# Kernel optimization log

Hardware: AMD Instinct MI355X
Metric: run time of the kernel (lower is better)

Reference implementation:

```python
import math
import jax, jax.numpy as jnp
import numpy as np

B, S, D, H = 4, 1024, 768, 12  # batch, seq, hidden, heads (ViT-Base)
HD = D // H                     # head size = 64
EPS = 1e-12                     # F.normalize eps


def setup_inputs() -> dict:
    key = jax.random.key(0)
    ks = jax.random.split(key, 7)
    s = 0.02
    return {
        "hidden_states": jax.random.normal(ks[0], (B, S, D), dtype=jnp.float32),
        "Wq": jax.random.normal(ks[1], (D, D), dtype=jnp.float32) * s,
        "bq": jax.random.normal(ks[2], (D,), dtype=jnp.float32) * s,
        "Wv": jax.random.normal(ks[3], (D, D), dtype=jnp.float32) * s,
        "bv": jax.random.normal(ks[4], (D,), dtype=jnp.float32) * s,
        "Wo": jax.random.normal(ks[5], (D, D), dtype=jnp.float32) * s,
        "bo": jax.random.normal(ks[6], (D,), dtype=jnp.float32) * s,
    }


def _split_heads(x):
    # [B,S,D] -> [B,H,S,hd]
    b, s, _ = x.shape
    return x.reshape(b, s, H, HD).transpose(0, 2, 1, 3)


def reference(hidden_states, Wq, bq, Wv, bv, Wo, bo):
    b, s, d_model = hidden_states.shape
    # Linear layers (torch Linear: x @ W^T + b; here W stored already transposed)
    mixed_q = hidden_states @ Wq + bq          # key == query in this module
    mixed_v = hidden_states @ Wv + bv
    q = _split_heads(mixed_q)                  # [B,H,S,hd]
    v = _split_heads(mixed_v)                  # [B,H,S,hd]

    # symmetric self-attention (Q @ Q^T)
    scores = jnp.einsum("bhsd,bhtd->bhst", q, q) / math.sqrt(HD)
    probs1 = jax.nn.softmax(scores, axis=-1)                 # [B,H,S,S]
    probs = 0.5 * (probs1 + probs1.transpose(0, 1, 3, 2))    # symmetrize

    # F.normalize(value_layer, dim=2): L2-normalize along the SEQUENCE axis
    vnorm = jnp.maximum(jnp.sqrt(jnp.sum(v * v, axis=2, keepdims=True)), EPS)
    V = v / vnorm                                            # [B,H,S,hd]

    # random-walk Laplacian: D^{-1}(D - P) = I - P / rowsum  (diag structure exploited,
    # same math as diag_embed + matmul in the original)
    dvec = probs.sum(axis=3)                                 # [B,H,S]
    Pn = probs / dvec[..., :, None]                          # D^{-1} P
    LrwV = V - jnp.einsum("bhst,bhtd->bhsd", Pn, V)          # L_rw @ V

    # trace( sum_{b,h} V^T L_rw V ) = sum over all (b,h,s,d) of V * (L_rw V)
    denom = jnp.float32(HD * H * b)
    tr = jnp.abs(jnp.sum(V * LrwV)) / denom

    # orthogonality regularizer: sum (V^T V - I)^2
    VtV = jnp.einsum("bhsd,bhse->bhde", V, V)                # [B,H,hd,hd]
    regular_term = jnp.sum((VtV - jnp.eye(HD, dtype=V.dtype)) ** 2) / denom

    # context = P @ V  (is_last=False)
    ctx = jnp.einsum("bhst,bhtd->bhsd", probs, v)
    ctx = ctx.transpose(0, 2, 1, 3).reshape(b, s, d_model)
    attention_output = ctx @ Wo + bo                         # dropout = identity (p=0)
    return (attention_output, tr, regular_term, mixed_q, mixed_q)
```

## Files before the change

### kernel.cpp

```cpp
#include <hip/hip_runtime.h>
#include <math.h>

constexpr float SCALE = 0.125f;

typedef __attribute__((ext_vector_type(8))) short bf8;
typedef __attribute__((ext_vector_type(8))) unsigned short u16x8;
typedef __attribute__((ext_vector_type(4))) float f32x4;

static __device__ __forceinline__ unsigned short f2bf(float f) {
    unsigned int u = __float_as_uint(f);
    u += 0x7fffu + ((u >> 16) & 1u);
    return (unsigned short)(u >> 16);
}
static __device__ __forceinline__ float bf2f(unsigned short h) {
    return __uint_as_float(((unsigned int)h) << 16);
}
static __device__ __forceinline__ bf8 ld8(const unsigned short* p) {
    return *reinterpret_cast<const bf8*>(p);
}
static __device__ __forceinline__ unsigned int cvtpk(float lo, float hi) {
    unsigned int r;
    asm("v_cvt_pk_bf16_f32 %0, %1, %2" : "=v"(r) : "v"(lo), "v"(hi));
    return r;
}

__global__ __launch_bounds__(256)
void k_prep(const float* __restrict__ Wq, const float* __restrict__ Wv,
            unsigned short* __restrict__ WTq, unsigned short* __restrict__ WTv)
{
    __shared__ unsigned short T[64 * 72];
    const int bid = blockIdx.x;
    const bool isQ = (bid < 144);
    const int lb = isQ ? bid : bid - 144;
    const float* __restrict__ W = isQ ? Wq : Wv;
    unsigned short* __restrict__ WT = isQ ? WTq : WTv;
    const int n0 = (lb % 12) * 64;
    const int k0 = (lb / 12) * 64;
    const int tid = threadIdx.x;
    const int r  = tid >> 2;
    const int c0 = (tid & 3) * 16;
    const float* src = &W[(size_t)(k0 + r) * 768 + n0 + c0];
    #pragma unroll
    for (int q = 0; q < 4; ++q) {
        const float4 v = *reinterpret_cast<const float4*>(src + q * 4);
        uint2 pk;
        pk.x = cvtpk(v.x, v.y);
        pk.y = cvtpk(v.z, v.w);
        *reinterpret_cast<uint2*>(&T[r * 72 + c0 + q * 4]) = pk;
    }
    __syncthreads();
    const int n  = tid >> 2;
    const int kc = (tid & 3) * 16;
    u16x8 o0, o1;
    #pragma unroll
    for (int i = 0; i < 8; ++i) o0[i] = T[(kc + i) * 72 + n];
    #pragma unroll
    for (int i = 0; i < 8; ++i) o1[i] = T[(kc + 8 + i) * 72 + n];
    unsigned short* dst = WT + (size_t)(n0 + n) * 768 + k0 + kc;
    *reinterpret_cast<u16x8*>(dst)     = o0;
    *reinterpret_cast<u16x8*>(dst + 8) = o1;
}

__global__ __launch_bounds__(256)
void k_gemm_qv(const float* __restrict__ X,
               const unsigned short* __restrict__ WTq,
               const unsigned short* __restrict__ WTv,
               const float* __restrict__ bq, const float* __restrict__ bv,
               float* __restrict__ mq1, float* __restrict__ mq2,
               unsigned short* __restrict__ qb, unsigned short* __restrict__ mvb)
{
    __shared__ unsigned short As[64 * 136];
    __shared__ unsigned short Bs[128 * 136];
    const int m0 = blockIdx.x * 64;
    const bool isQ = (blockIdx.y < 6);
    const int n0 = (isQ ? blockIdx.y : blockIdx.y - 6) * 128;
    const unsigned short* __restrict__ WT = isQ ? WTq : WTv;
    const float* __restrict__ bias = isQ ? bq : bv;
    const int tid = threadIdx.x;
    const int wave = tid >> 6, lane = tid & 63, lm = lane & 15, lg = lane >> 4;
    const int wn = wave;

    f32x4 acc[4][2];
    #pragma unroll
    for (int mi = 0; mi < 4; ++mi)
        #pragma unroll
        for (int ni = 0; ni < 2; ++ni) acc[mi][ni] = (f32x4){0.f, 0.f, 0.f, 0.f};

    float4 ar[8];
    u16x8  br[8];

    #pragma unroll
    for (int it = 0; it < 8; ++it) {
        const int idx = tid + it * 256;
        ar[it] = *reinterpret_cast<const float4*>(
            &X[(size_t)(m0 + (idx >> 5)) * 768 + (idx & 31) * 4]);
        br[it] = *reinterpret_cast<const u16x8*>(
            &WT[(size_t)(n0 + (idx >> 4)) * 768 + (idx & 15) * 8]);
    }
    #pragma unroll
    for (int it = 0; it < 8; ++it) {
        const int idx = tid + it * 256;
        uint2 pk;
        pk.x = cvtpk(ar[it].x, ar[it].y);
        pk.y = cvtpk(ar[it].z, ar[it].w);
        *reinterpret_cast<uint2*>(&As[(idx >> 5) * 136 + (idx & 31) * 4]) = pk;
        *reinterpret_cast<u16x8*>(&Bs[(idx >> 4) * 136 + (idx & 15) * 8]) = br[it];
    }
    __syncthreads();

    for (int step = 0; step < 6; ++step) {
        const bool pf = (step < 5);
        if (pf) {
            const int k0 = (step + 1) * 128;
            #pragma unroll
            for (int it = 0; it < 8; ++it) {
                const int idx = tid + it * 256;
                ar[it] = *reinterpret_cast<const float4*>(
                    &X[(size_t)(m0 + (idx >> 5)) * 768 + k0 + (idx & 31) * 4]);
                br[it] = *reinterpret_cast<const u16x8*>(
                    &WT[(size_t)(n0 + (idx >> 4)) * 768 + k0 + (idx & 15) * 8]);
            }
        }
        #pragma unroll
        for (int ks = 0; ks < 4; ++ks) {
            bf8 af[4], bfr[2];
            #pragma unroll
            for (int mi = 0; mi < 4; ++mi)
                af[mi] = *reinterpret_cast<const bf8*>(
                    &As[(mi * 16 + lm) * 136 + ks * 32 + lg * 8]);
            #pragma unroll
            for (int ni = 0; ni < 2; ++ni)
                bfr[ni] = *reinterpret_cast<const bf8*>(
                    &Bs[(wn * 32 + ni * 16 + lm) * 136 + ks * 32 + lg * 8]);
            #pragma unroll
            for (int mi = 0; mi < 4; ++mi)
                #pragma unroll
                for (int ni = 0; ni < 2; ++ni)
                    acc[mi][ni] = __builtin_amdgcn_mfma_f32_16x16x32_bf16(
                        af[mi], bfr[ni], acc[mi][ni], 0, 0, 0);
        }
        __syncthreads();
        if (pf) {
            #pragma unroll
            for (int it = 0; it < 8; ++it) {
                const int idx = tid + it * 256;
                uint2 pk;
                pk.x = cvtpk(ar[it].x, ar[it].y);
                pk.y = cvtpk(ar[it].z, ar[it].w);
                *reinterpret_cast<uint2*>(&As[(idx >> 5) * 136 + (idx & 31) * 4]) = pk;
                *reinterpret_cast<u16x8*>(&Bs[(idx >> 4) * 136 + (idx & 15) * 8]) = br[it];
            }
        }
        __syncthreads();
    }
    #pragma unroll
    for (int ni = 0; ni < 2; ++ni) {
        const int c = n0 + wn * 32 + ni * 16 + lm;
        const float bcol = bias[c];
        #pragma unroll
        for (int mi = 0; mi < 4; ++mi)
            #pragma unroll
            for (int j = 0; j < 4; ++j) {
                const int r = m0 + mi * 16 + lg * 4 + j;
                const float v = acc[mi][ni][j] + bcol;
                const size_t off = (size_t)r * 768 + c;
                if (isQ) {
                    mq1[off] = v;
                    mq2[off] = v;
                    qb[off]  = f2bf(v);
                } else {
                    mvb[off] = f2bf(v);
                }
            }
    }
}

__global__ __launch_bounds__(256)
void k_gemm_one(const unsigned short* __restrict__ Xb,
                const unsigned short* __restrict__ WT,
                const float* __restrict__ bias, float* __restrict__ out,
                const float* __restrict__ t1p, const float* __restrict__ t2p,
                const float* __restrict__ regp, float* __restrict__ out_tr,
                float* __restrict__ out_reg)
{
    __shared__ unsigned short As[64 * 136];
    __shared__ unsigned short Bs[64 * 136];
    __shared__ float R1[256];
    __shared__ float R2[256];
    __shared__ float R3[256];
    const int tid = threadIdx.x;

    if (blockIdx.x == 768) {
        float s1 = 0.f, s2 = 0.f, s3 = 0.f;
        for (int i = tid; i < 768; i += 256) s2 += t2p[i];
        if (tid < 48) { s1 = t1p[tid]; s3 = regp[tid]; }
        R1[tid] = s1; R2[tid] = s2; R3[tid] = s3;
        __syncthreads();
        for (int w = 128; w >= 1; w >>= 1) {
            if (tid < w) { R1[tid] += R1[tid + w]; R2[tid] += R2[tid + w]; R3[tid] += R3[tid + w]; }
            __syncthreads();
        }
        if (tid == 0) {
            *out_tr  = fabsf(R1[0] - R2[0]) / 3072.f;
            *out_reg = R3[0] / 3072.f;
        }
        return;
    }

    const int m0 = (blockIdx.x & 63) * 64;
    const int n0 = (blockIdx.x >> 6) * 64;
    const int w = tid >> 6, lane = tid & 63, lm = lane & 15, lg = lane >> 4;

    f32x4 acc[4];
    #pragma unroll
    for (int ni = 0; ni < 4; ++ni) acc[ni] = (f32x4){0.f, 0.f, 0.f, 0.f};

    u16x8 ara[4], arb[4];
    #pragma unroll
    for (int it = 0; it < 4; ++it) {
        const int idx = tid + it * 256;
        ara[it] = *reinterpret_cast<const u16x8*>(
            &Xb[(size_t)(m0 + (idx >> 4)) * 768 + (idx & 15) * 8]);
        arb[it] = *reinterpret_cast<const u16x8*>(
            &WT[(size_t)(n0 + (idx >> 4)) * 768 + (idx & 15) * 8]);
    }
    #pragma unroll
    for (int it = 0; it < 4; ++it) {
        const int idx = tid + it * 256;
        *reinterpret_cast<u16x8*>(&As[(idx >> 4) * 136 + (idx & 15) * 8]) = ara[it];
        *reinterpret_cast<u16x8*>(&Bs[(idx >> 4) * 136 + (idx & 15) * 8]) = arb[it];
    }
    __syncthreads();

    for (int step = 0; step < 6; ++step) {
        const bool pf = (step < 5);
        if (pf) {
            const int k0 = (step + 1) * 128;
            #pragma unroll
            for (int it = 0; it < 4; ++it) {
                const int idx = tid + it * 256;
                ara[it] = *reinterpret_cast<const u16x8*>(
                    &Xb[(size_t)(m0 + (idx >> 4)) * 768 + k0 + (idx & 15) * 8]);
                arb[it] = *reinterpret_cast<const u16x8*>(
                    &WT[(size_t)(n0 + (idx >> 4)) * 768 + k0 + (idx & 15) * 8]);
            }
        }
        #pragma unroll
        for (int ks = 0; ks < 4; ++ks) {
            const bf8 af = *reinterpret_cast<const bf8*>(
                &As[(w * 16 + lm) * 136 + ks * 32 + lg * 8]);
            #pragma unroll
            for (int ni = 0; ni < 4; ++ni) {
                const bf8 bfr = *reinterpret_cast<const bf8*>(
                    &Bs[(ni * 16 + lm) * 136 + ks * 32 + lg * 8]);
                acc[ni] = __builtin_amdgcn_mfma_f32_16x16x32_bf16(af, bfr, acc[ni], 0, 0, 0);
            }
        }
        __syncthreads();
        if (pf) {
            #pragma unroll
            for (int it = 0; it < 4; ++it) {
                const int idx = tid + it * 256;
                *reinterpret_cast<u16x8*>(&As[(idx >> 4) * 136 + (idx & 15) * 8]) = ara[it];
                *reinterpret_cast<u16x8*>(&Bs[(idx >> 4) * 136 + (idx & 15) * 8]) = arb[it];
            }
        }
        __syncthreads();
    }
    #pragma unroll
    for (int ni = 0; ni < 4; ++ni) {
        const int c = n0 + ni * 16 + lm;
        const float bcol = bias[c];
        #pragma unroll
        for (int j = 0; j < 4; ++j) {
            const int r = m0 + w * 16 + lg * 4 + j;
            out[(size_t)r * 768 + c] = acc[ni][j] + bcol;
        }
    }
}

__global__ __launch_bounds__(256)
void k_pass1T(const unsigned short* __restrict__ qb,
              const unsigned short* __restrict__ mvb,
              unsigned short* __restrict__ vT,
              float* __restrict__ a, float* __restrict__ nrmp)
{
    __shared__ __align__(16) unsigned short Kb[2][128 * 72];
    const int bid = blockIdx.x;
    const int st = (bid >> 3) & 15;
    const int bh = (bid & 7) + 8 * (bid >> 7);
    const int b = bh / 12, h = bh % 12;
    const int s0 = st * 64;
    const int tid = threadIdx.x;
    const int w = tid >> 6, lane = tid & 63, lm = lane & 15, lg = lane >> 4;
    const size_t qoff = (size_t)(b * 1024) * 768 + h * 64;

    {
        const int r  = tid >> 2;
        const int c0 = (tid & 3) * 16;
        const unsigned short* src = mvb + (size_t)(b * 1024 + s0 + r) * 768 + h * 64 + c0;
        const u16x8 x0 = *reinterpret_cast<const u16x8*>(src);
        const u16x8 x1 = *reinterpret_cast<const u16x8*>(src + 8);
        *reinterpret_cast<u16x8*>(&Kb[0][r * 72 + c0])     = x0;
        *reinterpret_cast<u16x8*>(&Kb[0][r * 72 + c0 + 8]) = x1;
        __syncthreads();
        const int dd  = tid >> 2;
        const int sc0 = (tid & 3) * 16;
        u16x8 o0, o1;
        float ps = 0.f;
        #pragma unroll
        for (int k = 0; k < 8; ++k) {
            o0[k] = Kb[0][(sc0 + k) * 72 + dd];
            const float v = bf2f(o0[k]);
            ps = fmaf(v, v, ps);
        }
        #pragma unroll
        for (int k = 0; k < 8; ++k) {
            o1[k] = Kb[0][(sc0 + 8 + k) * 72 + dd];
            const float v = bf2f(o1[k]);
            ps = fmaf(v, v, ps);
        }
        ps += __shfl_xor(ps, 1);
        ps += __shfl_xor(ps, 2);
        if ((tid & 3) == 0) nrmp[(size_t)(bh * 16 + st) * 64 + dd] = ps;
        unsigned short* dst = vT + (size_t)bh * 65536 + (size_t)dd * 1024 + s0 + sc0;
        *reinterpret_cast<u16x8*>(dst)     = o0;
        *reinterpret_cast<u16x8*>(dst + 8) = o1;
        __syncthreads();
    }

    const unsigned short* srow_p = qb + qoff + (size_t)(s0 + 16 * w + lm) * 768;
    const bf8 qs0 = ld8(srow_p + 8 * lg);
    const bf8 qs1 = ld8(srow_p + 32 + 8 * lg);
    const f32x4 z = {0.f, 0.f, 0.f, 0.f};
    float r = 0.f;

    u16x8 kr[4];
    #pragma unroll
    for (int it = 0; it < 4; ++it) {
        const int idx = tid + it * 256;
        kr[it] = *reinterpret_cast<const u16x8*>(
            qb + qoff + (size_t)(idx >> 3) * 768 + (idx & 7) * 8);
    }
    #pragma unroll
    for (int it = 0; it < 4; ++it) {
        const int idx = tid + it * 256;
        *reinterpret_cast<u16x8*>(&Kb[0][(idx >> 3) * 72 + (idx & 7) * 8]) = kr[it];
    }
    __syncthreads();
    int cur = 0;

    for (int tt = 0; tt < 8; ++tt) {
        const bool pf = (tt < 7);
        if (pf) {
            #pragma unroll
            for (int it = 0; it < 4; ++it) {
                const int idx = tid + it * 256;
                kr[it] = *reinterpret_cast<const u16x8*>(
                    qb + qoff + (size_t)((tt + 1) * 128 + (idx >> 3)) * 768 + (idx & 7) * 8);
            }
        }
        #pragma unroll
        for (int nf = 0; nf < 8; ++nf) {
            const bf8 ka0 = *reinterpret_cast<const bf8*>(
                &Kb[cur][(16 * nf + lm) * 72 + 8 * lg]);
            const bf8 ka1 = *reinterpret_cast<const bf8*>(
                &Kb[cur][(16 * nf + lm) * 72 + 32 + 8 * lg]);
            f32x4 ef = __builtin_amdgcn_mfma_f32_16x16x32_bf16(ka0, qs0, z, 0, 0, 0);
            ef = __builtin_amdgcn_mfma_f32_16x16x32_bf16(ka1, qs1, ef, 0, 0, 0);
            r += __expf(ef[0] * SCALE) + __expf(ef[1] * SCALE)
               + __expf(ef[2] * SCALE) + __expf(ef[3] * SCALE);
        }
        if (pf) {
            #pragma unroll
            for (int it = 0; it < 4; ++it) {
                const int idx = tid + it * 256;
                *reinterpret_cast<u16x8*>(
                    &Kb[cur ^ 1][(idx >> 3) * 72 + (idx & 7) * 8]) = kr[it];
            }
        }
        __syncthreads();
        cur ^= 1;
    }
    r += __shfl_xor(r, 16);
    r += __shfl_xor(r, 32);
    if (lg == 0) a[(size_t)bh * 1024 + s0 + 16 * w + lm] = 1.f / r;
}

__global__ __launch_bounds__(256)
void k_pass2(const unsigned short* __restrict__ qb,
             const unsigned short* __restrict__ vT,
             const unsigned short* __restrict__ mvb,
             const float* __restrict__ a,
             const float* __restrict__ nrmp,
             float* __restrict__ invn_out,
             unsigned short* __restrict__ ctxb,
             float* __restrict__ t2p)
{
    __shared__ __align__(16) unsigned short Kb[2][64 * 72];
    __shared__ __align__(16) unsigned short Vb[2][64 * 72];
    __shared__ __align__(16) unsigned short F_lds[4 * 16 * 72];
    __shared__ float red[256];
    __shared__ float inv_sh[64];
    const int bid = blockIdx.x;
    const int st = (bid >> 3) & 15;
    const int bh = (bid & 7) + 8 * (bid >> 7);
    const int b = bh / 12, h = bh % 12;
    const int s0 = st * 64;
    const int tid = threadIdx.x;
    const int w = tid >> 6, lane = tid & 63, lm = lane & 15, lg = lane >> 4;
    const size_t qoff = (size_t)(b * 1024) * 768 + h * 64;
    const unsigned short* srow_p = qb + qoff + (size_t)(s0 + 16 * w + lm) * 768;
    const bf8 qs0 = ld8(srow_p + 8 * lg);
    const bf8 qs1 = ld8(srow_p + 32 + 8 * lg);
    const unsigned short* vbase = vT + (size_t)bh * 65536;
    const float* abase = a + (size_t)bh * 1024;
    const float a_s = abase[s0 + 16 * w + lm];
    unsigned short* Frow = &F_lds[w * 1152 + lm * 72];
    const f32x4 z = {0.f, 0.f, 0.f, 0.f};
    f32x4 acc[4];
    #pragma unroll
    for (int nf = 0; nf < 4; ++nf) acc[nf] = z;
    float sF = 0.f;
    const int sr = tid >> 2;
    const int sc = (tid & 3) << 4;

    if (tid < 64) {
        float s = 0.f;
        #pragma unroll
        for (int t = 0; t < 16; ++t) s += nrmp[(size_t)(bh * 16 + t) * 64 + tid];
        const float iv = 1.f / fmaxf(sqrtf(s), 1e-12f);
        inv_sh[tid] = iv;
        if (st == 0) invn_out[bh * 64 + tid] = iv;
    }

    u16x8 kr0 = *reinterpret_cast<const u16x8*>(qb + qoff + (size_t)sr * 768 + sc);
    u16x8 kr1 = *reinterpret_cast<const u16x8*>(qb + qoff + (size_t)sr * 768 + sc + 8);
    u16x8 vr0 = *reinterpret_cast<const u16x8*>(vbase + (size_t)sr * 1024 + sc);
    u16x8 vr1 = *reinterpret_cast<const u16x8*>(vbase + (size_t)sr * 1024 + sc + 8);
    *reinterpret_cast<u16x8*>(&Kb[0][sr * 72 + sc])     = kr0;
    *reinterpret_cast<u16x8*>(&Kb[0][sr * 72 + sc + 8]) = kr1;
    *reinterpret_cast<u16x8*>(&Vb[0][sr * 72 + sc])     = vr0;
    *reinterpret_cast<u16x8*>(&Vb[0][sr * 72 + sc + 8]) = vr1;
    __syncthreads();
    int cur = 0;

    for (int tt = 0; tt < 16; ++tt) {
        const int t0 = tt * 64;
        if (tt < 15) {
            const size_t kg = qoff + (size_t)(t0 + 64 + sr) * 768 + sc;
            kr0 = *reinterpret_cast<const u16x8*>(qb + kg);
            kr1 = *reinterpret_cast<const u16x8*>(qb + kg + 8);
            const size_t vg = (size_t)sr * 1024 + t0 + 64 + sc;
            vr0 = *reinterpret_cast<const u16x8*>(vbase + vg);
            vr1 = *reinterpret_cast<const u16x8*>(vbase + vg + 8);
        }
        f32x4 ef[4];
        #pragma unroll
        for (int nf = 0; nf < 4; ++nf) {
            const bf8 ka0 = *reinterpret_cast<const bf8*>(
                &Kb[cur][(16 * nf + lm) * 72 + 8 * lg]);
            const bf8 ka1 = *reinterpret_cast<const bf8*>(
                &Kb[cur][(16 * nf + lm) * 72 + 32 + 8 * lg]);
            ef[nf] = __builtin_amdgcn_mfma_f32_16x16x32_bf16(ka0, qs0, z, 0, 0, 0);
            ef[nf] = __builtin_amdgcn_mfma_f32_16x16x32_bf16(ka1, qs1, ef[nf], 0, 0, 0);
        }
        #pragma unroll
        for (int nf = 0; nf < 4; ++nf) {
            const float4 af = *reinterpret_cast<const float4*>(
                abase + t0 + 16 * nf + 4 * lg);
            const float f0 = __expf(ef[nf][0] * SCALE) * (a_s + af.x);
            const float f1 = __expf(ef[nf][1] * SCALE) * (a_s + af.y);
            const float f2 = __expf(ef[nf][2] * SCALE) * (a_s + af.z);
            const float f3 = __expf(ef[nf][3] * SCALE) * (a_s + af.w);
            sF += (f0 + f1) + (f2 + f3);
            uint2 pk;
            pk.x = cvtpk(f0, f1);
            pk.y = cvtpk(f2, f3);
            *reinterpret_cast<uint2*>(&Frow[16 * nf + 4 * lg]) = pk;
        }
        #pragma unroll
        for (int ks = 0; ks < 2; ++ks) {
            const bf8 fa = *reinterpret_cast<const bf8*>(&Frow[32 * ks + 8 * lg]);
            #pragma unroll
            for (int nf = 0; nf < 4; ++nf) {
                const bf8 vfr = *reinterpret_cast<const bf8*>(
                    &Vb[cur][(16 * nf + lm) * 72 + 32 * ks + 8 * lg]);
                acc[nf] = __builtin_amdgcn_mfma_f32_16x16x32_bf16(fa, vfr, acc[nf], 0, 0, 0);
            }
        }
        if (tt < 15) {
            *reinterpret_cast<u16x8*>(&Kb[cur ^ 1][sr * 72 + sc])     = kr0;
            *reinterpret_cast<u16x8*>(&Kb[cur ^ 1][sr * 72 + sc + 8]) = kr1;
            *reinterpret_cast<u16x8*>(&Vb[cur ^ 1][sr * 72 + sc])     = vr0;
            *reinterpret_cast<u16x8*>(&Vb[cur ^ 1][sr * 72 + sc + 8]) = vr1;
        }
        __syncthreads();
        cur ^= 1;
    }
    sF += __shfl_xor(sF, 16);
    sF += __shfl_xor(sF, 32);

    float t2 = 0.f;
    #pragma unroll
    for (int j = 0; j < 4; ++j) {
        const int srow = s0 + 16 * w + 4 * lg + j;
        const float sFj = __shfl(sF, 4 * lg + j);
        const float rdv = 2.f / sFj;
        const size_t rowoff = (size_t)(b * 1024 + srow) * 768 + h * 64;
        #pragma unroll
        for (int nf = 0; nf < 4; ++nf) {
            const int d = lm + 16 * nf;
            const float iv = inv_sh[d];
            const float cf = 0.5f * acc[nf][j];
            ctxb[rowoff + d] = f2bf(cf);
            const float vv = bf2f(mvb[rowoff + d]);
            t2 = fmaf(vv * cf, iv * iv * rdv, t2);
        }
    }
    red[tid] = t2;
    __syncthreads();
    for (int k = 128; k >= 1; k >>= 1) {
        if (tid < k) red[tid] += red[tid + k];
        __syncthreads();
    }
    if (tid == 0) t2p[bh * 16 + st] = red[0];
}

__global__ __launch_bounds__(256)
void k_regwt(const unsigned short* __restrict__ vT, float* __restrict__ Gpart,
             const float* __restrict__ Wo, unsigned short* __restrict__ WTo)
{
    __shared__ unsigned short T[64 * 72];
    const int bid = blockIdx.x;
    const int tid = threadIdx.x;
    if (bid < 384) {
        const int bh = bid >> 3;
        const int q  = bid & 7;
        const int w = tid >> 6, lane = tid & 63, lm = lane & 15, lg = lane >> 4;
        const unsigned short* base = vT + (size_t)bh * 65536;
        const unsigned short* arowp = base + (size_t)(16 * w + lm) * 1024;
        const f32x4 z = {0.f, 0.f, 0.f, 0.f};
        f32x4 acc[4];
        #pragma unroll
        for (int nf = 0; nf < 4; ++nf) acc[nf] = z;
        #pragma unroll
        for (int kk = 0; kk < 4; ++kk) {
            const int t0 = (q * 4 + kk) * 32 + 8 * lg;
            const bf8 av = ld8(arowp + t0);
            #pragma unroll
            for (int nf = 0; nf < 4; ++nf) {
                const bf8 bv = ld8(base + (size_t)(lm + 16 * nf) * 1024 + t0);
                acc[nf] = __builtin_amdgcn_mfma_f32_16x16x32_bf16(av, bv, acc[nf], 0, 0, 0);
            }
        }
        float* gdst = Gpart + (size_t)(bh * 8 + q) * 4096;
        #pragma unroll
        for (int nf = 0; nf < 4; ++nf) {
            const int d2 = lm + 16 * nf;
            #pragma unroll
            for (int j = 0; j < 4; ++j) {
                const int d1 = 16 * w + 4 * lg + j;
                gdst[d1 * 64 + d2] = acc[nf][j];
            }
        }
    } else {
        const int lb = bid - 384;
        const int n0 = (lb % 12) * 64;
        const int k0 = (lb / 12) * 64;
        const int r  = tid >> 2;
        const int c0 = (tid & 3) * 16;
        const float* src = &Wo[(size_t)(k0 + r) * 768 + n0 + c0];
        #pragma unroll
        for (int q = 0; q < 4; ++q) {
            const float4 v = *reinterpret_cast<const float4*>(src + q * 4);
            uint2 pk;
            pk.x = cvtpk(v.x, v.y);
            pk.y = cvtpk(v.z, v.w);
            *reinterpret_cast<uint2*>(&T[r * 72 + c0 + q * 4]) = pk;
        }
        __syncthreads();
        const int n  = tid >> 2;
        const int kc = (tid & 3) * 16;
        u16x8 o0, o1;
        #pragma unroll
        for (int i = 0; i < 8; ++i) o0[i] = T[(kc + i) * 72 + n];
        #pragma unroll
        for (int i = 0; i < 8; ++i) o1[i] = T[(kc + 8 + i) * 72 + n];
        unsigned short* dst = WTo + (size_t)(n0 + n) * 768 + k0 + kc;
        *reinterpret_cast<u16x8*>(dst)     = o0;
        *reinterpret_cast<u16x8*>(dst + 8) = o1;
    }
}

__global__ __launch_bounds__(256)
void k_regfin(const float* __restrict__ Gpart, const float* __restrict__ invn,
              const float* __restrict__ nrmp,
              float* __restrict__ regp, float* __restrict__ t1p)
{
    const int bh = blockIdx.x;
    const int tid = threadIdx.x;
    float part = 0.f;
    for (int c = tid; c < 4096; c += 256) {
        const int d1 = c >> 6, d2 = c & 63;
        float g = 0.f;
        #pragma unroll
        for (int q = 0; q < 8; ++q)
            g += Gpart[(size_t)(bh * 8 + q) * 4096 + c];
        g *= invn[bh * 64 + d1] * invn[bh * 64 + d2];
        const float diff = g - ((d1 == d2) ? 1.f : 0.f);
        part = fmaf(diff, diff, part);
    }
    float t1l = 0.f;
    if (tid < 64) {
        float s = 0.f;
        #pragma unroll
        for (int t = 0; t < 16; ++t) s += nrmp[(size_t)(bh * 16 + t) * 64 + tid];
        const float iv = invn[bh * 64 + tid];
        t1l = s * iv * iv;
    }
    __shared__ float red[256];
    __shared__ float redT[256];
    red[tid] = part;
    redT[tid] = t1l;
    __syncthreads();
    for (int k = 128; k >= 1; k >>= 1) {
        if (tid < k) { red[tid] += red[tid + k]; redT[tid] += redT[tid + k]; }
        __syncthreads();
    }
    if (tid == 0) { regp[bh] = red[0]; t1p[bh] = redT[0]; }
}

extern "C" void kernel_launch(void* const* d_in, const int* in_sizes, int n_in,
                              void* d_out, int out_size, void* d_ws, size_t ws_size,
                              hipStream_t stream)
{
    const float* X  = (const float*)d_in[0];
    const float* Wq = (const float*)d_in[1];
    const float* bq = (const float*)d_in[2];
    const float* Wv = (const float*)d_in[3];
    const float* bv = (const float*)d_in[4];
    const float* Wo = (const float*)d_in[5];
    const float* bo = (const float*)d_in[6];

    float* out = (float*)d_out;
    float* att = out;
    float* tr  = out + 3145728;
    float* rg  = out + 3145729;
    float* mq1 = out + 3145730;
    float* mq2 = out + 6291458;

    float* ws = (float*)d_ws;
    unsigned short* mvb  = (unsigned short*)(ws);
    unsigned short* WTo  = (unsigned short*)(ws);
    unsigned short* qb   = (unsigned short*)(ws + 1572864);
    float*          Gpart = ws + 1572864;
    unsigned short* vTslot = (unsigned short*)(ws + 3145728);
    unsigned short* WTq  = vTslot;
    unsigned short* WTv  = vTslot + 589824;
    unsigned short* vT   = vTslot;
    unsigned short* ctxb = (unsigned short*)(ws + 4718592);
    float* nrmp = ws + 6291456;
    float* aarr = ws + 6389760;
    float* invn = ws + 6438960;
    float* t1p  = ws + 6442032;
    float* t2p  = ws + 6442080;
    float* regp = ws + 6442848;

    if (ws_size < (size_t)6442896 * sizeof(float)) return;

    k_prep     <<<288,          256, 0, stream>>>(Wq, Wv, WTq, WTv);
    k_gemm_qv  <<<dim3(64, 12), 256, 0, stream>>>(X, WTq, WTv, bq, bv, mq1, mq2, qb, mvb);
    k_pass1T   <<<768,          256, 0, stream>>>(qb, mvb, vT, aarr, nrmp);
    k_pass2    <<<768,          256, 0, stream>>>(qb, vT, mvb, aarr, nrmp, invn, ctxb, t2p);
    k_regwt    <<<528,          256, 0, stream>>>(vT, Gpart, Wo, WTo);
    k_regfin   <<<48,           256, 0, stream>>>(Gpart, invn, nrmp, regp, t1p);
    k_gemm_one <<<769,          256, 0, stream>>>(ctxb, WTo, bo, att,
                                                  t1p, t2p, regp, tr, rg);
}
```

Before: 123.0 us.

## Double-buffer LDS in projection GEMMs with smaller K tiles and more blocks

Both GEMM kernels now use two LDS buffers with a 64-wide K step, so the next tile is written to the other buffer while the current one is consumed. This drops one barrier per iteration. The QV GEMM tile also shrinks from 64x128 to 64x64, doubling the grid to 1536 blocks for better occupancy across CUs. The cost is twice as many K iterations, each with less MFMA work to hide global loads, and less operand reuse per block.

```diff
diff --git a/kernel.cpp b/kernel.cpp
--- a/kernel.cpp
+++ b/kernel.cpp
@@ -69,109 +69,113 @@
                float* __restrict__ mq1, float* __restrict__ mq2,
                unsigned short* __restrict__ qb, unsigned short* __restrict__ mvb)
 {
-    __shared__ unsigned short As[64 * 136];
-    __shared__ unsigned short Bs[128 * 136];
+    __shared__ __align__(16) unsigned short As[2][64 * 72];
+    __shared__ __align__(16) unsigned short Bs[2][64 * 72];
     const int m0 = blockIdx.x * 64;
-    const bool isQ = (blockIdx.y < 6);
-    const int n0 = (isQ ? blockIdx.y : blockIdx.y - 6) * 128;
+    const bool isQ = (blockIdx.y < 12);
+    const int n0 = (isQ ? blockIdx.y : blockIdx.y - 12) * 64;
     const unsigned short* __restrict__ WT = isQ ? WTq : WTv;
     const float* __restrict__ bias = isQ ? bq : bv;
     const int tid = threadIdx.x;
-    const int wave = tid >> 6, lane = tid & 63, lm = lane & 15, lg = lane >> 4;
-    const int wn = wave;
-
-    f32x4 acc[4][2];
-    #pragma unroll
-    for (int mi = 0; mi < 4; ++mi)
-        #pragma unroll
-        for (int ni = 0; ni < 2; ++ni) acc[mi][ni] = (f32x4){0.f, 0.f, 0.f, 0.f};
-
-    float4 ar[8];
-    u16x8  br[8];
-
-    #pragma unroll
-    for (int it = 0; it < 8; ++it) {
+    const int w = tid >> 6, lane = tid & 63, lm = lane & 15, lg = lane >> 4;
+
+    f32x4 acc[4];
+    #pragma unroll
+    for (int ni = 0; ni < 4; ++ni) acc[ni] = (f32x4){0.f, 0.f, 0.f, 0.f};
+
+    float4 ar[4];
+    u16x8  br[2];
+    #pragma unroll
+    for (int it = 0; it < 4; ++it) {
         const int idx = tid + it * 256;
         ar[it] = *reinterpret_cast<const float4*>(
-            &X[(size_t)(m0 + (idx >> 5)) * 768 + (idx & 31) * 4]);
+            &X[(size_t)(m0 + (idx >> 4)) * 768 + (idx & 15) * 4]);
+    }
+    #pragma unroll
+    for (int it = 0; it < 2; ++it) {
+        const int idx = tid + it * 256;
         br[it] = *reinterpret_cast<const u16x8*>(
-            &WT[(size_t)(n0 + (idx >> 4)) * 768 + (idx & 15) * 8]);
-    }
-    #pragma unroll
-    for (int it = 0; it < 8; ++it) {
+            &WT[(size_t)(n0 + (idx >> 3)) * 768 + (idx & 7) * 8]);
+    }
+    #pragma unroll
+    for (int it = 0; it < 4; ++it) {
         const int idx = tid + it * 256;
         uint2 pk;
         pk.x = cvtpk(ar[it].x, ar[it].y);
         pk.y = cvtpk(ar[it].z, ar[it].w);
-        *reinterpret_cast<uint2*>(&As[(idx >> 5) * 136 + (idx & 31) * 4]) = pk;
-        *reinterpret_cast<u16x8*>(&Bs[(idx >> 4) * 136 + (idx & 15) * 8]) = br[it];
+        *reinterpret_cast<uint2*>(&As[0][(idx >> 4) * 72 + (idx & 15) * 4]) = pk;
+    }
+    #pragma unroll
+    for (int it = 0; it < 2; ++it) {
+        const int idx = tid + it * 256;
+        *reinterpret_cast<u16x8*>(&Bs[0][(idx >> 3) * 72 + (idx & 7) * 8]) = br[it];
     }
     __syncthreads();
-
-    for (int step = 0; step < 6; ++step) {
-        const bool pf = (step < 5);
+    int cur = 0;
+
+    for (int step = 0; step < 12; ++step) {
+        const bool pf = (step < 11);
         if (pf) {
-            const int k0 = (step + 1) * 128;
-            #pragma unroll
-            for (int it = 0; it < 8; ++it) {
+            const int k0 = (step + 1) * 64;
+            #pragma unroll
+            for (int it = 0; it < 4; ++it) {
                 const int idx = tid + it * 256;
                 ar[it] = *reinterpret_cast<const float4*>(
-                    &X[(size_t)(m0 + (idx >> 5)) * 768 + k0 + (idx & 31) * 4]);
+                    &X[(size_t)(m0 + (idx >> 4)) * 768 + k0 + (idx & 15) * 4]);
+            }
+            #pragma unroll
+            for (int it = 0; it < 2; ++it) {
+                const int idx = tid + it * 256;
                 br[it] = *reinterpret_cast<const u16x8*>(
-                    &WT[(size_t)(n0 + (idx >> 4)) * 768 + k0 + (idx & 15) * 8]);
-            }
-        }
-        #pragma unroll
-        for (int ks = 0; ks < 4; ++ks) {
-            bf8 af[4], bfr[2];
-            #pragma unroll
-            for (int mi = 0; mi < 4; ++mi)
-                af[mi] = *reinterpret_cast<const bf8*>(
-                    &As[(mi * 16 + lm) * 136 + ks * 32 + lg * 8]);
-            #pragma unroll
-            for (int ni = 0; ni < 2; ++ni)
-                bfr[ni] = *reinterpret_cast<const bf8*>(
-                    &Bs[(wn * 32 + ni * 16 + lm) * 136 + ks * 32 + lg * 8]);
-            #pragma unroll
-            for (int mi = 0; mi < 4; ++mi)
-                #pragma unroll
-                for (int ni = 0; ni < 2; ++ni)
-                    acc[mi][ni] = __builtin_amdgcn_mfma_f32_16x16x32_bf16(
-                        af[mi], bfr[ni], acc[mi][ni], 0, 0, 0);
-        }
-        __syncthreads();
+                    &WT[(size_t)(n0 + (idx >> 3)) * 768 + k0 + (idx & 7) * 8]);
+            }
+        }
+        #pragma unroll
+        for (int ks = 0; ks < 2; ++ks) {
+            const bf8 af = *reinterpret_cast<const bf8*>(
+                &As[cur][(w * 16 + lm) * 72 + ks * 32 + lg * 8]);
+            #pragma unroll
+            for (int ni = 0; ni < 4; ++ni) {
+                const bf8 bfr = *reinterpret_cast<const bf8*>(
+                    &Bs[cur][(ni * 16 + lm) * 72 + ks * 32 + lg * 8]);
+                acc[ni] = __builtin_amdgcn_mfma_f32_16x16x32_bf16(af, bfr, acc[ni], 0, 0, 0);
+            }
+        }
         if (pf) {
             #pragma unroll
-            for (int it = 0; it < 8; ++it) {
+            for (int it = 0; it < 4; ++it) {
                 const int idx = tid + it * 256;
                 uint2 pk;
                 pk.x = cvtpk(ar[it].x, ar[it].y);
                 pk.y = cvtpk(ar[it].z, ar[it].w);
-                *reinterpret_cast<uint2*>(&As[(idx >> 5) * 136 + (idx & 31) * 4]) = pk;
-                *reinterpret_cast<u16x8*>(&Bs[(idx >> 4) * 136 + (idx & 15) * 8]) = br[it];
-            }
-        }
-        __syncthreads();
-    }
-    #pragma unroll
-    for (int ni = 0; ni < 2; ++ni) {
-        const int c = n0 + wn * 32 + ni * 16 + lm;
+                *reinterpret_cast<uint2*>(&As[cur ^ 1][(idx >> 4) * 72 + (idx & 15) * 4]) = pk;
+            }
+            #pragma unroll
+            for (int it = 0; it < 2; ++it) {
+                const int idx = tid + it * 256;
+                *reinterpret_cast<u16x8*>(&Bs[cur ^ 1][(idx >> 3) * 72 + (idx & 7) * 8]) = br[it];
+            }
+        }
+        __syncthreads();
+        cur ^= 1;
+    }
+    #pragma unroll
+    for (int ni = 0; ni < 4; ++ni) {
+        const int c = n0 + ni * 16 + lm;
         const float bcol = bias[c];
         #pragma unroll
-        for (int mi = 0; mi < 4; ++mi)
-            #pragma unroll
-            for (int j = 0; j < 4; ++j) {
-                const int r = m0 + mi * 16 + lg * 4 + j;
-                const float v = acc[mi][ni][j] + bcol;
-                const size_t off = (size_t)r * 768 + c;
-                if (isQ) {
-                    mq1[off] = v;
-                    mq2[off] = v;
-                    qb[off]  = f2bf(v);
-                } else {
-                    mvb[off] = f2bf(v);
-                }
-            }
+        for (int j = 0; j < 4; ++j) {
+            const int r = m0 + w * 16 + lg * 4 + j;
+            const float v = acc[ni][j] + bcol;
+            const size_t off = (size_t)r * 768 + c;
+            if (isQ) {
+                mq1[off] = v;
+                mq2[off] = v;
+                qb[off]  = f2bf(v);
+            } else {
+                mvb[off] = f2bf(v);
+            }
+        }
     }
 }
 
@@ -183,8 +187,8 @@
                 const float* __restrict__ regp, float* __restrict__ out_tr,
                 float* __restrict__ out_reg)
 {
-    __shared__ unsigned short As[64 * 136];
-    __shared__ unsigned short Bs[64 * 136];
+    __shared__ __align__(16) unsigned short As[2][64 * 72];
+    __shared__ __align__(16) unsigned short Bs[2][64 * 72];
     __shared__ float R1[256];
     __shared__ float R2[256];
     __shared__ float R3[256];
@@ -215,57 +219,58 @@
     #pragma unroll
     for (int ni = 0; ni < 4; ++ni) acc[ni] = (f32x4){0.f, 0.f, 0.f, 0.f};
 
-    u16x8 ara[4], arb[4];
-    #pragma unroll
-    for (int it = 0; it < 4; ++it) {
+    u16x8 ara[2], arb[2];
+    #pragma unroll
+    for (int it = 0; it < 2; ++it) {
         const int idx = tid + it * 256;
         ara[it] = *reinterpret_cast<const u16x8*>(
-            &Xb[(size_t)(m0 + (idx >> 4)) * 768 + (idx & 15) * 8]);
+            &Xb[(size_t)(m0 + (idx >> 3)) * 768 + (idx & 7) * 8]);
         arb[it] = *reinterpret_cast<const u16x8*>(
-            &WT[(size_t)(n0 + (idx >> 4)) * 768 + (idx & 15) * 8]);
-    }
-    #pragma unroll
-    for (int it = 0; it < 4; ++it) {
-        const int idx = tid + it * 256;
-        *reinterpret_cast<u16x8*>(&As[(idx >> 4) * 136 + (idx & 15) * 8]) = ara[it];
-        *reinterpret_cast<u16x8*>(&Bs[(idx >> 4) * 136 + (idx & 15) * 8]) = arb[it];
+            &WT[(size_t)(n0 + (idx >> 3)) * 768 + (idx & 7) * 8]);
+    }
+    #pragma unroll
+    for (int it = 0; it < 2; ++it) {
+        const int idx = tid + it * 256;
+        *reinterpret_cast<u16x8*>(&As[0][(idx >> 3) * 72 + (idx & 7) * 8]) = ara[it];
+        *reinterpret_cast<u16x8*>(&Bs[0][(idx >> 3) * 72 + (idx & 7) * 8]) = arb[it];
     }
     __syncthreads();
-
-    for (int step = 0; step < 6; ++step) {
-        const bool pf = (step < 5);
+    int cur = 0;
+
+    for (int step = 0; step < 12; ++step) {
+        const bool pf = (step < 11);
         if (pf) {
-            const int k0 = (step + 1) * 128;
-            #pragma unroll
-            for (int it = 0; it < 4; ++it) {
+            const int k0 = (step + 1) * 64;
+            #pragma unroll
+            for (int it = 0; it < 2; ++it) {
                 const int idx = tid + it * 256;
                 ara[it] = *reinterpret_cast<const u16x8*>(
-                    &Xb[(size_t)(m0 + (idx >> 4)) * 768 + k0 + (idx & 15) * 8]);
+                    &Xb[(size_t)(m0 + (idx >> 3)) * 768 + k0 + (idx & 7) * 8]);
                 arb[it] = *reinterpret_cast<const u16x8*>(
-                    &WT[(size_t)(n0 + (idx >> 4)) * 768 + k0 + (idx & 15) * 8]);
-            }
-        }
-        #pragma unroll
-        for (int ks = 0; ks < 4; ++ks) {
+                    &WT[(size_t)(n0 + (idx >> 3)) * 768 + k0 + (idx & 7) * 8]);
+            }
+        }
+        #pragma unroll
+        for (int ks = 0; ks < 2; ++ks) {
             const bf8 af = *reinterpret_cast<const bf8*>(
-                &As[(w * 16 + lm) * 136 + ks * 32 + lg * 8]);
+                &As[cur][(w * 16 + lm) * 72 + ks * 32 + lg * 8]);
             #pragma unroll
             for (int ni = 0; ni < 4; ++ni) {
                 const bf8 bfr = *reinterpret_cast<const bf8*>(
-                    &Bs[(ni * 16 + lm) * 136 + ks * 32 + lg * 8]);
+                    &Bs[cur][(ni * 16 + lm) * 72 + ks * 32 + lg * 8]);
                 acc[ni] = __builtin_amdgcn_mfma_f32_16x16x32_bf16(af, bfr, acc[ni], 0, 0, 0);
             }
         }
-        __syncthreads();
         if (pf) {
             #pragma unroll
-            for (int it = 0; it < 4; ++it) {
-                const int idx = tid + it * 256;
-                *reinterpret_cast<u16x8*>(&As[(idx >> 4) * 136 + (idx & 15) * 8]) = ara[it];
-                *reinterpret_cast<u16x8*>(&Bs[(idx >> 4) * 136 + (idx & 15) * 8]) = arb[it];
-            }
-        }
-        __syncthreads();
+            for (int it = 0; it < 2; ++it) {
+                const int idx = tid + it * 256;
+                *reinterpret_cast<u16x8*>(&As[cur ^ 1][(idx >> 3) * 72 + (idx & 7) * 8]) = ara[it];
+                *reinterpret_cast<u16x8*>(&Bs[cur ^ 1][(idx >> 3) * 72 + (idx & 7) * 8]) = arb[it];
+            }
+        }
+        __syncthreads();
+        cur ^= 1;
     }
     #pragma unroll
     for (int ni = 0; ni < 4; ++ni) {
@@ -670,7 +675,7 @@
     if (ws_size < (size_t)6442896 * sizeof(float)) return;
 
     k_prep     <<<288,          256, 0, stream>>>(Wq, Wv, WTq, WTv);
-    k_gemm_qv  <<<dim3(64, 12), 256, 0, stream>>>(X, WTq, WTv, bq, bv, mq1, mq2, qb, mvb);
+    k_gemm_qv  <<<dim3(64, 24), 256, 0, stream>>>(X, WTq, WTv, bq, bv, mq1, mq2, qb, mvb);
     k_pass1T   <<<768,          256, 0, stream>>>(qb, mvb, vT, aarr, nrmp);
     k_pass2    <<<768,          256, 0, stream>>>(qb, vT, mvb, aarr, nrmp, invn, ctxb, t2p);
     k_regwt    <<<528,          256, 0, stream>>>(vT, Gpart, Wo, WTo);
```

Result: no change. 124.5 us (+1.2%).
